# Kernel optimization log

Measured on AMD Instinct MI355X. Metric: run time of the kernel, lower is better.

Reference implementation:

```python
import jax, jax.numpy as jnp
import numpy as np

B, N, D = 2, 4096, 1152   # batch, tokens, txt_dim == pix_dim (num_heads = 1)
RMS_EPS = 1e-8


def setup_inputs() -> dict:
    key = jax.random.key(0)
    ks = jax.random.split(key, 8)
    w = lambda k, shape: jax.random.normal(k, shape, dtype=jnp.float32) * 0.02
    return {
        "x": jax.random.normal(ks[0], (B, N, D), dtype=jnp.float32),
        "c": jax.random.normal(ks[1], (B, N, D), dtype=jnp.float32),
        "Wqkv_pix": w(ks[2], (3 * D, D)),      # nn.Linear(pix_dim, 3*pix_dim), no bias
        "Wqkv_text": w(ks[3], (3 * D, D)),     # nn.Linear(txt_dim, 3*txt_dim), no bias
        "sq_text": jnp.ones((D,), jnp.float32),
        "sk_text": jnp.ones((D,), jnp.float32),
        "sq_pix": jnp.ones((D,), jnp.float32),
        "sk_pix": jnp.ones((D,), jnp.float32),
        "Wproj_pix": w(ks[4], (D, 2 * D)),     # nn.Linear(dim, txt_dim)
        "bproj_pix": jnp.zeros((D,), jnp.float32),
        "Wproj_text": w(ks[5], (D, 2 * D)),    # nn.Linear(dim, pix_dim)
        "bproj_text": jnp.zeros((D,), jnp.float32),
    }


def _rms_norm(t, scale):
    # RMSNorm with p<0 path: L2 norm over last dim, rms = ||x|| * d^-0.5
    d = t.shape[-1]
    rms = jnp.linalg.norm(t, axis=-1, keepdims=True) * (d ** -0.5)
    return scale * (t / (rms + RMS_EPS))


def reference(x, c, Wqkv_pix, Wqkv_text, sq_text, sk_text, sq_pix, sk_pix,
              Wproj_pix, bproj_pix, Wproj_text, bproj_text):
    Bx, Nx, D1 = x.shape  # num_heads == 1, so (B, 1, N, d) == (B, N, d)
    # pix stream QKV (from x)
    qkv_pix = (x @ Wqkv_pix.T).reshape(Bx, Nx, 3, D1)
    q_pix, k_pix, v_pix = qkv_pix[:, :, 0], qkv_pix[:, :, 1], qkv_pix[:, :, 2]
    q_pix = _rms_norm(q_pix, sq_pix)
    k_pix = _rms_norm(k_pix, sk_pix)
    # text stream QKV: NOTE the original code applies qkv_text to x, not c
    qkv_text = (x @ Wqkv_text.T).reshape(Bx, Nx, 3, D1)
    q_text, k_text, v_text = qkv_text[:, :, 0], qkv_text[:, :, 1], qkv_text[:, :, 2]
    q_text = _rms_norm(q_text, sq_text)
    k_text = _rms_norm(k_text, sk_text)
    # concat text/pix along feature dim -> (B, N, 2D)
    q = jnp.concatenate([q_text, q_pix], axis=-1)
    k = jnp.concatenate([k_text, k_pix], axis=-1)
    v = jnp.concatenate([v_text, v_pix], axis=-1)
    scale = (2 * D1) ** -0.5  # head_dim = (txt_dim + pix_dim) / num_heads
    attn = jax.nn.softmax(jnp.einsum("bnd,bmd->bnm", q, k) * scale, axis=-1)
    z = jnp.einsum("bnm,bmd->bnd", attn, v)  # (B, N, 2D)
    x_out = z @ Wproj_pix.T + bproj_pix
    c_out = z @ Wproj_text.T + bproj_text
    return (x_out, c_out)
```

## Files before the change

### kernel.cpp

```cpp
#include <hip/hip_runtime.h>
#include <hip/hip_bf16.h>
#include <stdint.h>

using short8 = __attribute__((ext_vector_type(8))) short;
using f32x4  = __attribute__((ext_vector_type(4))) float;

#define DD 1152
#define ROW 6912

static __device__ __forceinline__ float bf2f(uint32_t h){
  union { uint32_t u; float f; } v; v.u = (h & 0xffffu) << 16; return v.f;
}
static __device__ __forceinline__ ushort f2bf(float f){
  union { float f; uint32_t u; } v; v.f = f;
  uint32_t r = (v.u + 0x7fffu + ((v.u >> 16) & 1u)) >> 16;
  return (ushort)r;
}
static __device__ __forceinline__ uint32_t pack2(float a, float b){
  return (uint32_t)f2bf(a) | ((uint32_t)f2bf(b) << 16);
}

static __device__ __forceinline__ void gload16(const void* g, void* l){
  __builtin_amdgcn_global_load_lds(
      (const __attribute__((address_space(1))) void*)g,
      (__attribute__((address_space(3))) void*)l, 16, 0, 0);
}

template<int EPI>
__global__ __launch_bounds__(512, 2)
void gemmRP(const ushort* __restrict__ A, int lda, long long sA,
            const ushort* __restrict__ Bm, int ldb, long long sB,
            void* __restrict__ Cout, int ldc, long long sC,
            int K, float alpha, int ntx, int row0,
            float* __restrict__ out0, float* __restrict__ out1,
            const float* __restrict__ bias0, const float* __restrict__ bias1)
{
  __shared__ __align__(16) ushort lds[49152];
  const int tid  = threadIdx.x;
  const int w    = tid >> 6, lane = tid & 63;
  const int wr   = w >> 1, wc = w & 1;

  A  += (long long)blockIdx.y * sA;
  Bm += (long long)blockIdx.y * sB;

  const int nwg = gridDim.x;
  const int wg  = blockIdx.x;
  const int swz = (wg & 7) * (nwg >> 3) + (wg >> 3);
  const int tx = swz % ntx, ty = swz / ntx;
  const int m0 = ty * 256, n0 = tx * 128;

  const int srow = lane >> 2;
  const int scol = 8 * ((lane & 3) ^ ((lane >> 3) & 3));
  const ushort* gA0 = A  + (size_t)(m0 + (2 * w) * 16 + srow) * lda + scol;
  const ushort* gA1 = gA0 + (size_t)16 * lda;
  const ushort* gB0 = Bm + (size_t)(n0 + w * 16 + srow) * ldb + scol;

  auto stage = [&](int t, int bf) {
    ushort* Lb = lds + bf * 12288;
    gload16(gA0 + t * 32, Lb + (2 * w) * 512);
    gload16(gA1 + t * 32, Lb + (2 * w) * 512 + 512);
    gload16(gB0 + t * 32, Lb + 8192 + w * 512);
  };

  const int kq   = lane >> 4;
  const int rowA = wr * 64 + (lane & 15);
  const int adA  = rowA * 32 + 8 * (kq ^ ((rowA >> 1) & 3));
  const int rowB = wc * 64 + (lane & 15);
  const int adB  = 8192 + rowB * 32 + 8 * (kq ^ ((rowB >> 1) & 3));

  f32x4 acc[4][4];
#pragma unroll
  for (int m = 0; m < 4; m++)
#pragma unroll
    for (int n = 0; n < 4; n++) acc[m][n] = f32x4{0.f, 0.f, 0.f, 0.f};

  const int nt = K >> 5;

  short8 aP[4], bP[4], aQ[4], bQ[4];

  stage(0, 0); stage(1, 1); stage(2, 2);
  asm volatile("s_waitcnt vmcnt(3)" ::: "memory");
  __builtin_amdgcn_s_barrier();
#pragma unroll
  for (int m = 0; m < 4; m++) aP[m] = *(const short8*)(lds + adA + m * 512);
#pragma unroll
  for (int n = 0; n < 4; n++) bP[n] = *(const short8*)(lds + adB + n * 512);

  auto iter = [&](int t, short8 (&CA)[4], short8 (&CB)[4],
                         short8 (&NA)[4], short8 (&NB)[4]) {
    if (t + 1 < nt) {
      const ushort* Lb = lds + ((t + 1) & 3) * 12288;
#pragma unroll
      for (int m = 0; m < 4; m++) NA[m] = *(const short8*)(Lb + adA + m * 512);
#pragma unroll
      for (int n = 0; n < 4; n++) NB[n] = *(const short8*)(Lb + adB + n * 512);
    }
    if (t + 3 < nt) stage(t + 3, (t + 3) & 3);
    __builtin_amdgcn_s_setprio(1);
#pragma unroll
    for (int m = 0; m < 4; m++)
#pragma unroll
      for (int n = 0; n < 4; n++)
        acc[m][n] = __builtin_amdgcn_mfma_f32_16x16x32_bf16(CA[m], CB[n], acc[m][n], 0, 0, 0);
    __builtin_amdgcn_s_setprio(0);
    if (t + 3 < nt) asm volatile("s_waitcnt vmcnt(3)" ::: "memory");
    else            asm volatile("s_waitcnt vmcnt(0)" ::: "memory");
    __builtin_amdgcn_s_barrier();
  };

  for (int t = 0; t < nt; t += 2) {
    iter(t,     aP, bP, aQ, bQ);
    iter(t + 1, aQ, bQ, aP, bP);
  }

#pragma unroll
  for (int m = 0; m < 4; m++) {
#pragma unroll
    for (int v = 0; v < 4; v++) {
      const int row = m0 + wr * 64 + m * 16 + (lane >> 4) * 4 + v;
#pragma unroll
      for (int n = 0; n < 4; n++) {
        const int col = n0 + wc * 64 + n * 16 + (lane & 15);
        float val = acc[m][n][v] * alpha;
        if (EPI == 0) {
          ((ushort*)Cout)[(long long)blockIdx.y * sC + (size_t)row * ldc + col] = f2bf(val);
        } else {
          const int orow = row0 + row;
          if (col < DD) out0[(size_t)orow * DD + col] = val + bias0[col];
          else          out1[(size_t)orow * DD + (col - DD)] = val + bias1[col - DD];
        }
      }
    }
  }
}

__global__ __launch_bounds__(256)
void cvt_f32_bf16(const float* __restrict__ src, ushort* __restrict__ dst, int n4)
{
  int stride = gridDim.x * blockDim.x;
  for (int i = blockIdx.x * blockDim.x + threadIdx.x; i < n4; i += stride) {
    float4 v = ((const float4*)src)[i];
    uint2 o;
    o.x = pack2(v.x, v.y);
    o.y = pack2(v.z, v.w);
    ((uint2*)dst)[i] = o;
  }
}

__global__ __launch_bounds__(256)
void rms_inplace(ushort* __restrict__ qkv,
                 const float* __restrict__ sq_text, const float* __restrict__ sq_pix,
                 const float* __restrict__ sk_text, const float* __restrict__ sk_pix)
{
  const int row = blockIdx.x;
  const int tid = threadIdx.x, wave = tid >> 6, lane = tid & 63;
  ushort* seg = qkv + (size_t)row * ROW + wave * 1152;
  const float* scale = (wave == 0) ? sq_text : (wave == 1) ? sq_pix
                     : (wave == 2) ? sk_text : sk_pix;
  float ss = 0.f;
  for (int g = lane; g < 144; g += 64) {
    uint4 p = *(const uint4*)(seg + g * 8);
    float f0 = bf2f(p.x), f1 = bf2f(p.x >> 16), f2 = bf2f(p.y), f3 = bf2f(p.y >> 16);
    float f4 = bf2f(p.z), f5 = bf2f(p.z >> 16), f6 = bf2f(p.w), f7 = bf2f(p.w >> 16);
    ss += f0*f0 + f1*f1 + f2*f2 + f3*f3 + f4*f4 + f5*f5 + f6*f6 + f7*f7;
  }
#pragma unroll
  for (int off = 32; off; off >>= 1) ss += __shfl_xor(ss, off);
  float rms = sqrtf(ss) * 0.0294627825f;
  float inv = 1.0f / (rms + 1e-8f);
  for (int g = lane; g < 144; g += 64) {
    int d0 = g * 8;
    uint4 p = *(const uint4*)(seg + d0);
    float f[8];
    f[0]=bf2f(p.x); f[1]=bf2f(p.x>>16); f[2]=bf2f(p.y); f[3]=bf2f(p.y>>16);
    f[4]=bf2f(p.z); f[5]=bf2f(p.z>>16); f[6]=bf2f(p.w); f[7]=bf2f(p.w>>16);
    uint4 o;
    o.x = pack2(f[0]*scale[d0+0]*inv, f[1]*scale[d0+1]*inv);
    o.y = pack2(f[2]*scale[d0+2]*inv, f[3]*scale[d0+3]*inv);
    o.z = pack2(f[4]*scale[d0+4]*inv, f[5]*scale[d0+5]*inv);
    o.w = pack2(f[6]*scale[d0+6]*inv, f[7]*scale[d0+7]*inv);
    *(uint4*)(seg + d0) = o;
  }
}

__global__ __launch_bounds__(256)
void transpose_v(const ushort* __restrict__ qkv, ushort* __restrict__ Vt)
{
  __shared__ ushort t[64][72];
  const int nb = blockIdx.x, db = blockIdx.y, b = blockIdx.z;
  const int tid = threadIdx.x;
  const int d0 = db * 64;
  const int srccol = 4608 + d0;
  const int rr = tid >> 3, cc = (tid & 7) * 8;
#pragma unroll
  for (int it = 0; it < 2; it++) {
    int r = rr + it * 32;
    uint4 p = *(const uint4*)(qkv + (size_t)(b * 4096 + nb * 64 + r) * ROW + srccol + cc);
    *(uint4*)&t[r][cc] = p;
  }
  __syncthreads();
#pragma unroll
  for (int it = 0; it < 2; it++) {
    int d = rr + it * 32;
    uint4 o;
    o.x = (uint32_t)t[cc+0][d] | ((uint32_t)t[cc+1][d] << 16);
    o.y = (uint32_t)t[cc+2][d] | ((uint32_t)t[cc+3][d] << 16);
    o.z = (uint32_t)t[cc+4][d] | ((uint32_t)t[cc+5][d] << 16);
    o.w = (uint32_t)t[cc+6][d] | ((uint32_t)t[cc+7][d] << 16);
    *(uint4*)(Vt + ((size_t)b * 2304 + d0 + d) * 4096 + nb * 64 + cc) = o;
  }
}

__global__ __launch_bounds__(256)
void softmax_bf16(ushort* __restrict__ S)
{
  const int row = blockIdx.x;
  ushort* sr = S + (size_t)row * 4096;
  const int tid = threadIdx.x, wave = tid >> 6, lane = tid & 63;
  __shared__ float red[8];
  uint4 p0 = ((const uint4*)sr)[tid * 2];
  uint4 p1 = ((const uint4*)sr)[tid * 2 + 1];
  float f[16];
  f[0]=bf2f(p0.x); f[1]=bf2f(p0.x>>16); f[2]=bf2f(p0.y); f[3]=bf2f(p0.y>>16);
  f[4]=bf2f(p0.z); f[5]=bf2f(p0.z>>16); f[6]=bf2f(p0.w); f[7]=bf2f(p0.w>>16);
  f[8]=bf2f(p1.x); f[9]=bf2f(p1.x>>16); f[10]=bf2f(p1.y); f[11]=bf2f(p1.y>>16);
  f[12]=bf2f(p1.z); f[13]=bf2f(p1.z>>16); f[14]=bf2f(p1.w); f[15]=bf2f(p1.w>>16);
  float mx = f[0];
#pragma unroll
  for (int j = 1; j < 16; j++) mx = fmaxf(mx, f[j]);
#pragma unroll
  for (int off = 32; off; off >>= 1) mx = fmaxf(mx, __shfl_xor(mx, off));
  if (lane == 0) red[wave] = mx;
  __syncthreads();
  mx = fmaxf(fmaxf(red[0], red[1]), fmaxf(red[2], red[3]));
  float s = 0.f;
#pragma unroll
  for (int j = 0; j < 16; j++) { f[j] = expf(f[j] - mx); s += f[j]; }
#pragma unroll
  for (int off = 32; off; off >>= 1) s += __shfl_xor(s, off);
  if (lane == 0) red[4 + wave] = s;
  __syncthreads();
  s = red[4] + red[5] + red[6] + red[7];
  float inv = 1.0f / s;
  uint4 o0, o1;
  o0.x = pack2(f[0]*inv, f[1]*inv);  o0.y = pack2(f[2]*inv, f[3]*inv);
  o0.z = pack2(f[4]*inv, f[5]*inv);  o0.w = pack2(f[6]*inv, f[7]*inv);
  o1.x = pack2(f[8]*inv, f[9]*inv);  o1.y = pack2(f[10]*inv, f[11]*inv);
  o1.z = pack2(f[12]*inv, f[13]*inv); o1.w = pack2(f[14]*inv, f[15]*inv);
  ((uint4*)sr)[tid * 2]     = o0;
  ((uint4*)sr)[tid * 2 + 1] = o1;
}

extern "C" void kernel_launch(void* const* d_in, const int* in_sizes, int n_in,
                              void* d_out, int out_size, void* d_ws, size_t ws_size,
                              hipStream_t stream)
{
  const float* x          = (const float*)d_in[0];
  const float* Wqkv_pix   = (const float*)d_in[2];
  const float* Wqkv_text  = (const float*)d_in[3];
  const float* sq_text    = (const float*)d_in[4];
  const float* sk_text    = (const float*)d_in[5];
  const float* sq_pix     = (const float*)d_in[6];
  const float* sk_pix     = (const float*)d_in[7];
  const float* Wproj_pix  = (const float*)d_in[8];
  const float* bproj_pix  = (const float*)d_in[9];
  const float* Wproj_text = (const float*)d_in[10];
  const float* bproj_text = (const float*)d_in[11];

  if (ws_size < 195166208ULL) return;
  char* ws = (char*)d_ws;
  ushort* QKV = (ushort*)(ws);
  ushort* S1  = (ushort*)(ws);
  ushort* Z   = (ushort*)(ws + 33554432);
  ushort* Vt  = (ushort*)(ws + 113246208);
  ushort* S0  = (ushort*)(ws + 150994944);
  ushort* Wpb = (ushort*)(ws + 184549376);
  ushort* xb  = (ushort*)(ws + 113246208);
  ushort* Wb  = (ushort*)(ws + 150994944);

  cvt_f32_bf16<<<2048, 256, 0, stream>>>(x, xb, 9437184 / 4);
  for (int t = 0; t < 3; t++) {
    cvt_f32_bf16<<<512, 256, 0, stream>>>(Wqkv_text + (size_t)t * 1327104,
                                          Wb + (size_t)(2 * t) * 1327104, 1327104 / 4);
    cvt_f32_bf16<<<512, 256, 0, stream>>>(Wqkv_pix + (size_t)t * 1327104,
                                          Wb + (size_t)(2 * t + 1) * 1327104, 1327104 / 4);
  }
  cvt_f32_bf16<<<512, 256, 0, stream>>>(Wproj_pix, Wpb, 2654208 / 4);
  cvt_f32_bf16<<<512, 256, 0, stream>>>(Wproj_text, Wpb + 2654208, 2654208 / 4);

  gemmRP<0><<<dim3(1728), 512, 0, stream>>>(xb, 1152, 0, Wb, 1152, 0, QKV, ROW, 0,
                                            1152, 1.0f, 54, 0,
                                            nullptr, nullptr, nullptr, nullptr);
  rms_inplace<<<8192, 256, 0, stream>>>(QKV, sq_text, sq_pix, sk_text, sk_pix);
  {
    dim3 g(64, 36, 2);
    transpose_v<<<g, 256, 0, stream>>>(QKV, Vt);
  }

  const float scale = 1.0f / 48.0f;
  const size_t slab = (size_t)4096 * ROW;

  gemmRP<0><<<dim3(512), 512, 0, stream>>>(QKV, ROW, 0, QKV + 2304, ROW, 0,
                                           S0, 4096, 0, 2304, scale, 32, 0,
                                           nullptr, nullptr, nullptr, nullptr);
  softmax_bf16<<<4096, 256, 0, stream>>>(S0);
  gemmRP<0><<<dim3(512), 512, 0, stream>>>(QKV + slab, ROW, 0, QKV + slab + 2304, ROW, 0,
                                           S1, 4096, 0, 2304, scale, 32, 0,
                                           nullptr, nullptr, nullptr, nullptr);
  softmax_bf16<<<4096, 256, 0, stream>>>(S1);

  {
    long long sAb = (long long)(S1 - S0);
    long long sBb = (long long)2304 * 4096;
    long long sCb = (long long)4096 * 2304;
    gemmRP<0><<<dim3(288, 2), 512, 0, stream>>>(S0, 4096, sAb, Vt, 4096, sBb,
                                                Z, 2304, sCb, 4096, 1.0f, 18, 0,
                                                nullptr, nullptr, nullptr, nullptr);
  }

  {
    float* out0 = (float*)d_out;
    float* out1 = out0 + 9437184;
    gemmRP<2><<<dim3(576), 512, 0, stream>>>(Z, 2304, 0, Wpb, 2304, 0, nullptr, 0, 0,
                                             2304, 1.0f, 18, 0,
                                             out0, out1, bproj_pix, bproj_text);
  }
}
```

Measured before the change: 805.4 us.

## Deepen GEMM LDS ring to five stages and barrier once per two k-steps

Restructures the shared bf16 GEMM main loop from a 4-buffer ring with prefetch distance 3 to a 5-buffer ring with prefetch distance 4. The loop is manually unrolled by two with rotating buffer indices, so the vmcnt wait and workgroup barrier happen once every two k-tiles instead of every tile. The goal is to hide more global-load latency and cut synchronisation overhead. LDS per block grows to 120 KB, which likely drops occupancy from two blocks per CU to one. A TAG template parameter gives each GEMM launch its own instantiation.

```diff
diff --git a/kernel.cpp b/kernel.cpp
--- a/kernel.cpp
+++ b/kernel.cpp
@@ -26,7 +26,7 @@
       (__attribute__((address_space(3))) void*)l, 16, 0, 0);
 }
 
-template<int EPI>
+template<int EPI, int TAG>
 __global__ __launch_bounds__(512, 2)
 void gemmRP(const ushort* __restrict__ A, int lda, long long sA,
             const ushort* __restrict__ Bm, int ldb, long long sB,
@@ -35,7 +35,7 @@
             float* __restrict__ out0, float* __restrict__ out1,
             const float* __restrict__ bias0, const float* __restrict__ bias1)
 {
-  __shared__ __align__(16) ushort lds[49152];
+  __shared__ __align__(16) ushort lds[61440];
   const int tid  = threadIdx.x;
   const int w    = tid >> 6, lane = tid & 63;
   const int wr   = w >> 1, wc = w & 1;
@@ -78,39 +78,58 @@
 
   short8 aP[4], bP[4], aQ[4], bQ[4];
 
-  stage(0, 0); stage(1, 1); stage(2, 2);
+  stage(0, 0); stage(1, 1); stage(2, 2); stage(3, 3);
   asm volatile("s_waitcnt vmcnt(3)" ::: "memory");
   __builtin_amdgcn_s_barrier();
 #pragma unroll
   for (int m = 0; m < 4; m++) aP[m] = *(const short8*)(lds + adA + m * 512);
 #pragma unroll
   for (int n = 0; n < 4; n++) bP[n] = *(const short8*)(lds + adB + n * 512);
-
-  auto iter = [&](int t, short8 (&CA)[4], short8 (&CB)[4],
-                         short8 (&NA)[4], short8 (&NB)[4]) {
+  __builtin_amdgcn_s_barrier();
+
+  int b1 = 1;
+  int b4 = 4;
+
+  for (int t = 0; t < nt; t += 2) {
     if (t + 1 < nt) {
-      const ushort* Lb = lds + ((t + 1) & 3) * 12288;
-#pragma unroll
-      for (int m = 0; m < 4; m++) NA[m] = *(const short8*)(Lb + adA + m * 512);
-#pragma unroll
-      for (int n = 0; n < 4; n++) NB[n] = *(const short8*)(Lb + adB + n * 512);
+      const ushort* Lb = lds + b1 * 12288;
+#pragma unroll
+      for (int m = 0; m < 4; m++) aQ[m] = *(const short8*)(Lb + adA + m * 512);
+#pragma unroll
+      for (int n = 0; n < 4; n++) bQ[n] = *(const short8*)(Lb + adB + n * 512);
     }
-    if (t + 3 < nt) stage(t + 3, (t + 3) & 3);
+    if (t + 4 < nt) stage(t + 4, b4);
     __builtin_amdgcn_s_setprio(1);
 #pragma unroll
     for (int m = 0; m < 4; m++)
 #pragma unroll
       for (int n = 0; n < 4; n++)
-        acc[m][n] = __builtin_amdgcn_mfma_f32_16x16x32_bf16(CA[m], CB[n], acc[m][n], 0, 0, 0);
+        acc[m][n] = __builtin_amdgcn_mfma_f32_16x16x32_bf16(aP[m], bP[n], acc[m][n], 0, 0, 0);
     __builtin_amdgcn_s_setprio(0);
-    if (t + 3 < nt) asm volatile("s_waitcnt vmcnt(3)" ::: "memory");
+    b1++; if (b1 == 5) b1 = 0;
+    b4++; if (b4 == 5) b4 = 0;
+
+    if (t + 2 < nt) {
+      const ushort* Lb = lds + b1 * 12288;
+#pragma unroll
+      for (int m = 0; m < 4; m++) aP[m] = *(const short8*)(Lb + adA + m * 512);
+#pragma unroll
+      for (int n = 0; n < 4; n++) bP[n] = *(const short8*)(Lb + adB + n * 512);
+    }
+    if (t + 5 < nt) stage(t + 5, b4);
+    __builtin_amdgcn_s_setprio(1);
+#pragma unroll
+    for (int m = 0; m < 4; m++)
+#pragma unroll
+      for (int n = 0; n < 4; n++)
+        acc[m][n] = __builtin_amdgcn_mfma_f32_16x16x32_bf16(aQ[m], bQ[n], acc[m][n], 0, 0, 0);
+    __builtin_amdgcn_s_setprio(0);
+    b1++; if (b1 == 5) b1 = 0;
+    b4++; if (b4 == 5) b4 = 0;
+
+    if (t + 5 < nt) asm volatile("s_waitcnt vmcnt(3)" ::: "memory");
     else            asm volatile("s_waitcnt vmcnt(0)" ::: "memory");
     __builtin_amdgcn_s_barrier();
-  };
-
-  for (int t = 0; t < nt; t += 2) {
-    iter(t,     aP, bP, aQ, bQ);
-    iter(t + 1, aQ, bQ, aP, bP);
   }
 
 #pragma unroll
@@ -288,9 +307,9 @@
   cvt_f32_bf16<<<512, 256, 0, stream>>>(Wproj_pix, Wpb, 2654208 / 4);
   cvt_f32_bf16<<<512, 256, 0, stream>>>(Wproj_text, Wpb + 2654208, 2654208 / 4);
 
-  gemmRP<0><<<dim3(1728), 512, 0, stream>>>(xb, 1152, 0, Wb, 1152, 0, QKV, ROW, 0,
-                                            1152, 1.0f, 54, 0,
-                                            nullptr, nullptr, nullptr, nullptr);
+  gemmRP<0, 1><<<dim3(1728), 512, 0, stream>>>(xb, 1152, 0, Wb, 1152, 0, QKV, ROW, 0,
+                                               1152, 1.0f, 54, 0,
+                                               nullptr, nullptr, nullptr, nullptr);
   rms_inplace<<<8192, 256, 0, stream>>>(QKV, sq_text, sq_pix, sk_text, sk_pix);
   {
     dim3 g(64, 36, 2);
@@ -300,29 +319,29 @@
   const float scale = 1.0f / 48.0f;
   const size_t slab = (size_t)4096 * ROW;
 
-  gemmRP<0><<<dim3(512), 512, 0, stream>>>(QKV, ROW, 0, QKV + 2304, ROW, 0,
-                                           S0, 4096, 0, 2304, scale, 32, 0,
-                                           nullptr, nullptr, nullptr, nullptr);
+  gemmRP<0, 2><<<dim3(512), 512, 0, stream>>>(QKV, ROW, 0, QKV + 2304, ROW, 0,
+                                              S0, 4096, 0, 2304, scale, 32, 0,
+                                              nullptr, nullptr, nullptr, nullptr);
   softmax_bf16<<<4096, 256, 0, stream>>>(S0);
-  gemmRP<0><<<dim3(512), 512, 0, stream>>>(QKV + slab, ROW, 0, QKV + slab + 2304, ROW, 0,
-                                           S1, 4096, 0, 2304, scale, 32, 0,
-                                           nullptr, nullptr, nullptr, nullptr);
+  gemmRP<0, 2><<<dim3(512), 512, 0, stream>>>(QKV + slab, ROW, 0, QKV + slab + 2304, ROW, 0,
+                                              S1, 4096, 0, 2304, scale, 32, 0,
+                                              nullptr, nullptr, nullptr, nullptr);
   softmax_bf16<<<4096, 256, 0, stream>>>(S1);
 
   {
     long long sAb = (long long)(S1 - S0);
     long long sBb = (long long)2304 * 4096;
     long long sCb = (long long)4096 * 2304;
-    gemmRP<0><<<dim3(288, 2), 512, 0, stream>>>(S0, 4096, sAb, Vt, 4096, sBb,
-                                                Z, 2304, sCb, 4096, 1.0f, 18, 0,
-                                                nullptr, nullptr, nullptr, nullptr);
+    gemmRP<0, 3><<<dim3(288, 2), 512, 0, stream>>>(S0, 4096, sAb, Vt, 4096, sBb,
+                                                   Z, 2304, sCb, 4096, 1.0f, 18, 0,
+                                                   nullptr, nullptr, nullptr, nullptr);
   }
 
   {
     float* out0 = (float*)d_out;
     float* out1 = out0 + 9437184;
-    gemmRP<2><<<dim3(576), 512, 0, stream>>>(Z, 2304, 0, Wpb, 2304, 0, nullptr, 0, 0,
-                                             2304, 1.0f, 18, 0,
-                                             out0, out1, bproj_pix, bproj_text);
-  }
-}
+    gemmRP<2, 4><<<dim3(576), 512, 0, stream>>>(Z, 2304, 0, Wpb, 2304, 0, nullptr, 0, 0,
+                                                2304, 1.0f, 18, 0,
+                                                out0, out1, bproj_pix, bproj_text);
+  }
+}
```

Result: faster. 770.2 us (-4.4%).
